# Kernel tuning notes

Hardware: AMD Instinct MI355X
Metric: run time of the kernel (lower is better)

The kernel has to match this reference:

```python
import jax, jax.numpy as jnp
import numpy as np

D = 1024        # model dim (== moe_inter_dim, required by Expert's x2*x3)
H = 1024        # expert hidden dim (moe_inter_dim)
E = 8           # n_routed_experts
K = 2           # n_activated_experts (top-k)
I = 2 * 1024    # shared-expert inter dim = n_shared_experts * moe_inter_dim
ROUTE_SCALE = 1.0


def setup_inputs() -> dict:
    key = jax.random.key(0)
    ks = jax.random.split(key, 12)
    s = lambda *sh: 1.0 / np.sqrt(sh[-1])
    return {
        "x":      jax.random.normal(ks[0], (1, 2048, D), jnp.float32),
        "gate_w": jax.random.normal(ks[1], (E, D), jnp.float32) * s(E, D),
        "w1":     jax.random.normal(ks[2], (E, H, D), jnp.float32) * s(H, D),
        "b1":     jax.random.normal(ks[3], (E, H), jnp.float32) * 0.01,
        "w2":     jax.random.normal(ks[4], (E, D, H), jnp.float32) * s(D, H),
        "b2":     jax.random.normal(ks[5], (E, D), jnp.float32) * 0.01,
        "w3":     jax.random.normal(ks[6], (E, H, D), jnp.float32) * s(H, D),
        "b3":     jax.random.normal(ks[7], (E, H), jnp.float32) * 0.01,
        "sw1":    jax.random.normal(ks[8], (I, D), jnp.float32) * s(I, D),
        "sw2":    jax.random.normal(ks[9], (I, D), jnp.float32) * s(I, D),
        "sw3":    jax.random.normal(ks[10], (D, I), jnp.float32) * s(D, I),
    }


def reference(x, gate_w, w1, b1, w2, b2, w3, b3, sw1, sw2, sw3):
    B, S, _ = x.shape
    xt = x.reshape(-1, D)                                  # (T, D)
    # ---- Gate (softmax scoring, n_groups==1, no bias, route_scale=1) ----
    logits = xt @ gate_w.T                                 # (T, E)
    scores = jax.nn.softmax(logits.astype(jnp.float32), axis=-1)
    top_vals, idx = jax.lax.top_k(scores, K)               # (T, K)
    weights = (jnp.take_along_axis(scores, idx, axis=1)
               .astype(x.dtype)) * ROUTE_SCALE             # (T, K)
    # ---- Routed experts: input is scaled by routing weight BEFORE expert ----
    xs = xt[:, None, :] * weights[:, :, None]              # (T, K, D)
    y = jnp.zeros_like(xt)
    for e in range(E):  # fixed small loop over experts (dense masked dispatch)
        mask = (idx == e).astype(x.dtype)                  # (T, K)
        h = jax.nn.silu(jnp.einsum('tkd,hd->tkh', xs, w1[e]) + b1[e])
        x2 = jnp.einsum('tkh,dh->tkd', h, w2[e]) + b2[e]   # (T, K, D)
        x3 = jnp.einsum('tkd,hd->tkh', xs, w3[e]) + b3[e]  # (T, K, H==D)
        y = y + jnp.sum((x2 * x3) * mask[:, :, None], axis=1)
    # ---- Shared experts (SwiGLU MLP, no biases) ----
    z = (jax.nn.silu(xt @ sw1.T) * (xt @ sw2.T)) @ sw3.T   # (T, D)
    return (y + z).reshape(B, S, D)
```

## Files before the change

### kernel.cpp

```cpp
#include <hip/hip_runtime.h>

typedef unsigned short u16;
typedef __attribute__((ext_vector_type(4))) float floatx4;
typedef __attribute__((ext_vector_type(8))) short short8;

#define MAXROWS 5120
#define MAXMT 40

__device__ __forceinline__ u16 f2bf(float f) {
    union { float f; unsigned u; } v; v.f = f;
    unsigned r = v.u + 0x7FFF + ((v.u >> 16) & 1);
    return (u16)(r >> 16);
}
__device__ __forceinline__ float bf2f(u16 h) {
    union { unsigned u; float f; } v; v.u = ((unsigned)h) << 16; return v.f;
}
__device__ __forceinline__ float silu_f(float x) { return x / (1.f + __expf(-x)); }

__device__ __forceinline__ void gl_lds16(const void* g, void* l) {
    __builtin_amdgcn_global_load_lds(
        (__attribute__((address_space(1))) unsigned int*)g,
        (__attribute__((address_space(3))) unsigned int*)l, 16, 0, 0);
}

__global__ void conv_gate(const float* __restrict__ w1, const float* __restrict__ w2,
                          const float* __restrict__ w3, const float* __restrict__ sw1,
                          const float* __restrict__ sw2, const float* __restrict__ sw3,
                          const float* __restrict__ x, const float* __restrict__ gw,
                          u16* __restrict__ W13, u16* __restrict__ W2b,
                          u16* __restrict__ S12, u16* __restrict__ S3b,
                          u16* __restrict__ Xb,
                          int* __restrict__ idxA, float* __restrict__ wA) {
    int bid = blockIdx.x;
    if (bid < 512) {
        int w = threadIdx.x >> 6, lane = threadIdx.x & 63;
        int t = bid * 4 + w;
        const float* xr = x + (size_t)t * 1024;
        float acc[8];
#pragma unroll
        for (int e = 0; e < 8; e++) acc[e] = 0.f;
#pragma unroll
        for (int i = 0; i < 16; i++) {
            float xv = xr[lane + (i << 6)];
#pragma unroll
            for (int e = 0; e < 8; e++) acc[e] += xv * gw[e * 1024 + lane + (i << 6)];
        }
#pragma unroll
        for (int e = 0; e < 8; e++)
            for (int off = 32; off > 0; off >>= 1) acc[e] += __shfl_xor(acc[e], off);
        if (lane == 0) {
            float m = acc[0];
#pragma unroll
            for (int e = 1; e < 8; e++) m = fmaxf(m, acc[e]);
            float p[8], s = 0.f;
#pragma unroll
            for (int e = 0; e < 8; e++) { p[e] = __expf(acc[e] - m); s += p[e]; }
            float inv = 1.f / s;
#pragma unroll
            for (int e = 0; e < 8; e++) p[e] *= inv;
            int i0 = 0;
#pragma unroll
            for (int e = 1; e < 8; e++) if (p[e] > p[i0]) i0 = e;
            int i1 = (i0 == 0) ? 1 : 0;
            for (int e = i1 + 1; e < 8; e++) if (e != i0 && p[e] > p[i1]) i1 = e;
            idxA[2 * t] = i0; idxA[2 * t + 1] = i1;
            wA[2 * t] = p[i0]; wA[2 * t + 1] = p[i1];
        }
        return;
    }
    long j = (long)(bid - 512) * 256 + threadIdx.x;
    const float* src; u16* dst; long d;
    if (j < 2097152) {
        long e = j >> 18; src = w1; dst = W13; d = j + (e << 18);
    } else if ((j -= 2097152) < 2097152) {
        long e = j >> 18; src = w3; dst = W13; d = j + (e << 18) + 262144;
    } else if ((j -= 2097152) < 2097152) { src = w2;  dst = W2b; d = j; }
    else if ((j -= 2097152) < 524288) {
        long rr = j >> 8, c4 = j & 255;
        long br = ((rr >> 4) << 5) + (rr & 15);
        src = sw1; dst = S12; d = (br << 8) + c4;
    } else if ((j -= 524288) < 524288) {
        long rr = j >> 8, c4 = j & 255;
        long br = ((rr >> 4) << 5) + 16 + (rr & 15);
        src = sw2; dst = S12; d = (br << 8) + c4;
    } else if ((j -= 524288) < 524288)     { src = sw3; dst = S3b; d = j; }
    else { j -= 524288; src = x; dst = Xb; d = j; }
    float4 v = ((const float4*)src)[j];
    ushort4 o; o.x = f2bf(v.x); o.y = f2bf(v.y); o.z = f2bf(v.z); o.w = f2bf(v.w);
    ((ushort4*)dst)[d] = o;
}

__global__ void rank_k(const int* __restrict__ idxA, int* __restrict__ tileexp,
                       int* __restrict__ ntiles, int* __restrict__ slot_of) {
    int lane = threadIdx.x;
    const int* my = idxA + lane * 64;
    int h[8];
#pragma unroll
    for (int e = 0; e < 8; e++) h[e] = 0;
    for (int i = 0; i < 64; i++) {
        int v = my[i];
#pragma unroll
        for (int e = 0; e < 8; e++) h[e] += (v == e);
    }
    int excl[8], tot[8];
#pragma unroll
    for (int e = 0; e < 8; e++) {
        int inc = h[e];
        for (int off = 1; off < 64; off <<= 1) {
            int up = __shfl_up(inc, off);
            if (lane >= off) inc += up;
        }
        excl[e] = inc - h[e];
        tot[e] = __shfl(inc, 63);
    }
    int base[8], tiles = 0;
#pragma unroll
    for (int e = 0; e < 8; e++) {
        base[e] = tiles * 128;
        tiles += (tot[e] + 127) >> 7;
    }
    if (lane == 0) {
        ntiles[0] = tiles;
        int t = 0;
        for (int e = 0; e < 8; e++) {
            int te = (tot[e] + 127) >> 7;
            for (int j = 0; j < te; j++) tileexp[t++] = e;
        }
    }
    int c[8];
#pragma unroll
    for (int e = 0; e < 8; e++) c[e] = base[e] + excl[e];
    for (int i = 0; i < 64; i++) {
        int v = my[i], slot = 0;
#pragma unroll
        for (int e = 0; e < 8; e++) slot += (v == e) ? c[e] : 0;
#pragma unroll
        for (int e = 0; e < 8; e++) c[e] += (v == e);
        slot_of[lane * 64 + i] = slot;
    }
}

__global__ void build_xs(const float* __restrict__ x, const float* __restrict__ wA,
                         const int* __restrict__ slot_of, u16* __restrict__ XS) {
    int s = blockIdx.x, i = threadIdx.x;
    int t = s >> 1; float w = wA[s]; int slot = slot_of[s];
    float4 v = ((const float4*)(x + (size_t)t * 1024))[i];
    ushort4 o; o.x = f2bf(v.x * w); o.y = f2bf(v.y * w); o.z = f2bf(v.z * w); o.w = f2bf(v.w * w);
    ((ushort4*)(XS + (size_t)slot * 1024))[i] = o;
}

#define STAGE64(Ab, Bb, lda)                                                        \
    {                                                                               \
        _Pragma("unroll")                                                           \
        for (int t = 0; t < 2; t++) {                                               \
            int b = w + (t << 2);                                                   \
            int r = (b << 4) + rloc;                                                \
            int cg = clds ^ ((r >> 1) & 3);                                         \
            _Pragma("unroll")                                                       \
            for (int hh = 0; hh < 2; hh++) {                                        \
                gl_lds16(Ab + (size_t)(m0 + r) * lda + k0 + (hh << 5) + (cg << 3),  \
                         &ldsA[(b * 2 + hh) * 512]);                                \
                gl_lds16(Bb + (size_t)(n0 + r) * lda + k0 + (hh << 5) + (cg << 3),  \
                         &ldsB[(b * 2 + hh) * 512]);                                \
            }                                                                       \
        }                                                                           \
    }

#define MFMA64()                                                                    \
    {                                                                               \
        _Pragma("unroll")                                                           \
        for (int hh = 0; hh < 2; hh++) {                                            \
            short8 af[4], bf[4];                                                    \
            _Pragma("unroll")                                                       \
            for (int i = 0; i < 4; i++) {                                           \
                int rr = (wm << 6) + (i << 4) + l15;                                \
                int g = q ^ ((rr >> 1) & 3);                                        \
                af[i] = *(const short8*)&ldsA[((rr >> 4) * 2 + hh) * 512 +          \
                                              (rr & 15) * 32 + (g << 3)];           \
            }                                                                       \
            _Pragma("unroll")                                                       \
            for (int j = 0; j < 4; j++) {                                           \
                int rr = (wn << 6) + (j << 4) + l15;                                \
                int g = q ^ ((rr >> 1) & 3);                                        \
                bf[j] = *(const short8*)&ldsB[((rr >> 4) * 2 + hh) * 512 +          \
                                              (rr & 15) * 32 + (g << 3)];           \
            }                                                                       \
            _Pragma("unroll")                                                       \
            for (int i = 0; i < 4; i++)                                             \
                _Pragma("unroll")                                                   \
                for (int j = 0; j < 4; j++)                                         \
                    acc[i][j] = __builtin_amdgcn_mfma_f32_16x16x32_bf16(            \
                        af[i], bf[j], acc[i][j], 0, 0, 0);                          \
        }                                                                           \
    }

__global__ __launch_bounds__(256) void gemm_A(
    const u16* __restrict__ XS, const u16* __restrict__ Xb,
    const u16* __restrict__ W13, const u16* __restrict__ S12,
    const float* __restrict__ b1, const float* __restrict__ b3,
    u16* __restrict__ H, u16* __restrict__ X3h, u16* __restrict__ G,
    const int* __restrict__ tileexp, const int* __restrict__ ntiles) {
    __shared__ u16 ldsA[128 * 64];
    __shared__ u16 ldsB[128 * 64];
    int xcd = blockIdx.x & 7, ws = blockIdx.x >> 3;
    const u16 *Ab, *Bb; int mt, nt, e = 0; bool routed;
    if (ws < 80) {
        routed = true;
        mt = xcd * 5 + (ws >> 4);
        nt = ws & 15;
        if (mt >= ntiles[0]) return;
        e = tileexp[mt];
        Ab = XS; Bb = W13 + ((size_t)e << 21);
    } else {
        routed = false; int s = ws - 80;
        mt = ((xcd >> 2) << 3) + (s >> 3);
        nt = ((xcd & 3) << 3) + (s & 7);
        Ab = Xb; Bb = S12;
    }
    int m0 = mt * 128, n0 = nt * 128;
    int tid = threadIdx.x, w = tid >> 6, lane = tid & 63;
    int wm = w >> 1, wn = w & 1;

    floatx4 acc[4][4];
#pragma unroll
    for (int i = 0; i < 4; i++)
#pragma unroll
        for (int j = 0; j < 4; j++) { floatx4 z = {0.f, 0.f, 0.f, 0.f}; acc[i][j] = z; }

    int rloc = lane >> 2, clds = lane & 3, q = lane >> 4, l15 = lane & 15;

    for (int k0 = 0; k0 < 1024; k0 += 64) {
        STAGE64(Ab, Bb, 1024);
        __syncthreads();
        MFMA64();
        __syncthreads();
    }

    if (routed) {
#pragma unroll
        for (int i = 0; i < 4; i++) {
            int rowb = m0 + (wm << 6) + (i << 4) + (q << 2);
#pragma unroll
            for (int j = 0; j < 4; j++) {
                int col = n0 + (wn << 6) + (j << 4) + l15;
#pragma unroll
                for (int r = 0; r < 4; r++) {
                    float v = acc[i][j][r];
                    int rw = rowb + r;
                    if (nt < 8) {
                        H[(size_t)rw * 1024 + col] = f2bf(silu_f(v + b1[e * 1024 + col]));
                    } else {
                        int c2 = col - 1024;
                        X3h[(size_t)rw * 1024 + c2] = f2bf(v + b3[e * 1024 + c2]);
                    }
                }
            }
        }
    } else {
#pragma unroll
        for (int i = 0; i < 4; i++) {
            int rowb = m0 + (wm << 6) + (i << 4) + (q << 2);
#pragma unroll
            for (int jp = 0; jp < 4; jp += 2) {
                int brb = n0 + (wn << 6) + (jp << 4);
                int lcol = ((brb >> 5) << 4) + l15;
#pragma unroll
                for (int r = 0; r < 4; r++) {
                    float u = acc[i][jp][r], v = acc[i][jp + 1][r];
                    G[(size_t)(rowb + r) * 2048 + lcol] = f2bf(silu_f(u) * v);
                }
            }
        }
    }
}

__global__ __launch_bounds__(256) void gemm_B(
    const u16* __restrict__ H, const u16* __restrict__ G,
    const u16* __restrict__ W2b, const u16* __restrict__ S3b,
    const float* __restrict__ b2, const u16* __restrict__ X3h,
    u16* __restrict__ P0, u16* __restrict__ P1,
    float* __restrict__ Z0, float* __restrict__ Z1,
    const int* __restrict__ tileexp, const int* __restrict__ ntiles) {
    __shared__ u16 ldsA[128 * 64];
    __shared__ u16 ldsB[128 * 64];
    int xcd = blockIdx.x & 7, ws = blockIdx.x >> 3;
    const u16 *Ab, *Bb; int mt, nt, kc, lda, kbeg, kspan, e = 0; bool routed;
    if (ws < 80) {
        routed = true;
        mt = xcd * 5 + (ws >> 4);
        int r = ws & 15; nt = r & 7; kc = r >> 3;
        if (mt >= ntiles[0]) return;
        e = tileexp[mt];
        Ab = H; Bb = W2b + ((size_t)e << 20); lda = 1024; kbeg = kc << 9; kspan = 512;
    } else {
        routed = false; int s = ws - 80;
        kc = s & 1; int s2 = s >> 1;
        mt = ((xcd >> 1) << 2) + (s2 >> 2);
        nt = ((xcd & 1) << 2) + (s2 & 3);
        Ab = G; Bb = S3b; lda = 2048; kbeg = kc << 10; kspan = 1024;
    }
    int kend = kbeg + kspan;
    int m0 = mt * 128, n0 = nt * 128;
    int tid = threadIdx.x, w = tid >> 6, lane = tid & 63;
    int wm = w >> 1, wn = w & 1;

    floatx4 acc[4][4];
#pragma unroll
    for (int i = 0; i < 4; i++)
#pragma unroll
        for (int j = 0; j < 4; j++) { floatx4 z = {0.f, 0.f, 0.f, 0.f}; acc[i][j] = z; }

    int rloc = lane >> 2, clds = lane & 3, q = lane >> 4, l15 = lane & 15;

    for (int k0 = kbeg; k0 < kend; k0 += 64) {
        STAGE64(Ab, Bb, lda);
        __syncthreads();
        MFMA64();
        __syncthreads();
    }

    if (routed) {
        u16* Pk = kc ? P1 : P0;
#pragma unroll
        for (int i = 0; i < 4; i++) {
            int rowb = m0 + (wm << 6) + (i << 4) + (q << 2);
#pragma unroll
            for (int j = 0; j < 4; j++) {
                int col = n0 + (wn << 6) + (j << 4) + l15;
#pragma unroll
                for (int r = 0; r < 4; r++) {
                    int rw = rowb + r;
                    float v = acc[i][j][r] + (kc == 0 ? b2[e * 1024 + col] : 0.f);
                    float pv = v * bf2f(X3h[(size_t)rw * 1024 + col]);
                    Pk[(size_t)rw * 1024 + col] = f2bf(pv);
                }
            }
        }
    } else {
        float* Zk = kc ? Z1 : Z0;
#pragma unroll
        for (int i = 0; i < 4; i++) {
            int rowb = m0 + (wm << 6) + (i << 4) + (q << 2);
#pragma unroll
            for (int j = 0; j < 4; j++) {
                int col = n0 + (wn << 6) + (j << 4) + l15;
#pragma unroll
                for (int r = 0; r < 4; r++)
                    Zk[(size_t)(rowb + r) * 1024 + col] = acc[i][j][r];
            }
        }
    }
}

__global__ void final_k(const float* __restrict__ Z0, const float* __restrict__ Z1,
                        const u16* __restrict__ P0, const u16* __restrict__ P1,
                        const int* __restrict__ slot_of, float* __restrict__ out) {
    int i = blockIdx.x * 256 + threadIdx.x;
    int t = i >> 8, c4 = i & 255;
    int s0 = slot_of[2 * t], s1 = slot_of[2 * t + 1];
    float4 z0 = ((const float4*)Z0)[(size_t)t * 256 + c4];
    float4 z1 = ((const float4*)Z1)[(size_t)t * 256 + c4];
    ushort4 a0 = ((const ushort4*)P0)[(size_t)s0 * 256 + c4];
    ushort4 a1 = ((const ushort4*)P1)[(size_t)s0 * 256 + c4];
    ushort4 c0 = ((const ushort4*)P0)[(size_t)s1 * 256 + c4];
    ushort4 c1 = ((const ushort4*)P1)[(size_t)s1 * 256 + c4];
    float4 o;
    o.x = z0.x + z1.x + bf2f(a0.x) + bf2f(a1.x) + bf2f(c0.x) + bf2f(c1.x);
    o.y = z0.y + z1.y + bf2f(a0.y) + bf2f(a1.y) + bf2f(c0.y) + bf2f(c1.y);
    o.z = z0.z + z1.z + bf2f(a0.z) + bf2f(a1.z) + bf2f(c0.z) + bf2f(c1.z);
    o.w = z0.w + z1.w + bf2f(a0.w) + bf2f(a1.w) + bf2f(c0.w) + bf2f(c1.w);
    ((float4*)out)[(size_t)t * 256 + c4] = o;
}

extern "C" void kernel_launch(void* const* d_in, const int* in_sizes, int n_in,
                              void* d_out, int out_size, void* d_ws, size_t ws_size,
                              hipStream_t stream) {
    const float* x   = (const float*)d_in[0];
    const float* gw  = (const float*)d_in[1];
    const float* w1  = (const float*)d_in[2];
    const float* b1  = (const float*)d_in[3];
    const float* w2  = (const float*)d_in[4];
    const float* b2  = (const float*)d_in[5];
    const float* w3  = (const float*)d_in[6];
    const float* b3  = (const float*)d_in[7];
    const float* sw1 = (const float*)d_in[8];
    const float* sw2 = (const float*)d_in[9];
    const float* sw3 = (const float*)d_in[10];
    float* out = (float*)d_out;

    char* p = (char*)d_ws;
    int* ntiles  = (int*)(p + 192);
    int* tileexp = (int*)(p + 256);
    size_t off = 4096;
    u16*   XS      = (u16*)(p + off);   off += (size_t)MAXROWS * 1024 * 2;
    int*   idxA    = (int*)(p + off);   off += 16384;
    float* wA      = (float*)(p + off); off += 16384;
    int*   slot_of = (int*)(p + off);   off += 16384;
    u16*   H       = (u16*)(p + off);   off += (size_t)MAXROWS * 1024 * 2;
    u16*   X3h     = (u16*)(p + off);   off += (size_t)MAXROWS * 1024 * 2;
    u16*   P0      = (u16*)(p + off);   off += (size_t)MAXROWS * 1024 * 2;
    u16*   P1      = (u16*)(p + off);   off += (size_t)MAXROWS * 1024 * 2;
    float* Z0      = (float*)(p + off); off += (size_t)2048 * 1024 * 4;
    float* Z1      = (float*)(p + off); off += (size_t)2048 * 1024 * 4;
    u16*   W13     = (u16*)(p + off);   off += (size_t)8 * 2048 * 1024 * 2;
    u16*   W2b     = (u16*)(p + off);   off += (size_t)8 * 1024 * 1024 * 2;
    u16*   S12     = (u16*)(p + off);   off += (size_t)4096 * 1024 * 2;
    u16*   S3b     = (u16*)(p + off);   off += (size_t)1024 * 2048 * 2;
    u16*   Xb      = (u16*)(p + off);   off += (size_t)2048 * 1024 * 2;
    u16*   G       = (u16*)(p + off);   off += (size_t)2048 * 2048 * 2;

    conv_gate<<<33280, 256, 0, stream>>>(w1, w2, w3, sw1, sw2, sw3, x, gw,
                                         W13, W2b, S12, S3b, Xb, idxA, wA);
    rank_k<<<1, 64, 0, stream>>>(idxA, tileexp, ntiles, slot_of);
    build_xs<<<4096, 256, 0, stream>>>(x, wA, slot_of, XS);

    gemm_A<<<1152, 256, 0, stream>>>(XS, Xb, W13, S12, b1, b3, H, X3h, G,
                                     tileexp, ntiles);
    gemm_B<<<896, 256, 0, stream>>>(H, G, W2b, S3b, b2, X3h, P0, P1, Z0, Z1,
                                    tileexp, ntiles);
    final_k<<<2048, 256, 0, stream>>>(Z0, Z1, P0, P1, slot_of, out);
}
```

Before: 316.1 us.

## Double-buffer LDS staging of K=32 slices to overlap global loads with MFMA

Replaces the single-buffer K=64 stage/compute loop in both GEMM kernels with a two-buffer K=32 pipeline. The next slice is issued via global_load_lds while the current one feeds MFMAs, using explicit vmcnt waits and raw barriers. Fragment reads are done in inline asm with precomputed LDS addresses and a single lgkmcnt wait. LDS footprint stays at 32 KB, but barriers per K-step increase, and the hand-coded waitcnt values must match the number of in-flight loads.

```diff
diff --git a/kernel.cpp b/kernel.cpp
--- a/kernel.cpp
+++ b/kernel.cpp
@@ -22,6 +22,31 @@
         (__attribute__((address_space(1))) unsigned int*)g,
         (__attribute__((address_space(3))) unsigned int*)l, 16, 0, 0);
 }
+
+__device__ __forceinline__ void ld_frags(
+    unsigned a0, unsigned a1, unsigned a2, unsigned a3,
+    unsigned b0, unsigned b1, unsigned b2, unsigned b3,
+    short8& af0, short8& af1, short8& af2, short8& af3,
+    short8& bf0, short8& bf1, short8& bf2, short8& bf3) {
+    asm volatile(
+        "ds_read_b128 %0, %8\n\t"
+        "ds_read_b128 %1, %9\n\t"
+        "ds_read_b128 %2, %10\n\t"
+        "ds_read_b128 %3, %11\n\t"
+        "ds_read_b128 %4, %12\n\t"
+        "ds_read_b128 %5, %13\n\t"
+        "ds_read_b128 %6, %14\n\t"
+        "ds_read_b128 %7, %15\n\t"
+        "s_waitcnt lgkmcnt(0)"
+        : "=&v"(af0), "=&v"(af1), "=&v"(af2), "=&v"(af3),
+          "=&v"(bf0), "=&v"(bf1), "=&v"(bf2), "=&v"(bf3)
+        : "v"(a0), "v"(a1), "v"(a2), "v"(a3),
+          "v"(b0), "v"(b1), "v"(b2), "v"(b3));
+}
+
+#define WAIT_VM4() __builtin_amdgcn_s_waitcnt(3956)
+#define WAIT_VM0() __builtin_amdgcn_s_waitcnt(3952)
+#define BAR()      __builtin_amdgcn_s_barrier()
 
 __global__ void conv_gate(const float* __restrict__ w1, const float* __restrict__ w2,
                           const float* __restrict__ w3, const float* __restrict__ sw1,
@@ -149,50 +174,81 @@
     ((ushort4*)(XS + (size_t)slot * 1024))[i] = o;
 }
 
-#define STAGE64(Ab, Bb, lda)                                                        \
-    {                                                                               \
-        _Pragma("unroll")                                                           \
-        for (int t = 0; t < 2; t++) {                                               \
-            int b = w + (t << 2);                                                   \
-            int r = (b << 4) + rloc;                                                \
-            int cg = clds ^ ((r >> 1) & 3);                                         \
-            _Pragma("unroll")                                                       \
-            for (int hh = 0; hh < 2; hh++) {                                        \
-                gl_lds16(Ab + (size_t)(m0 + r) * lda + k0 + (hh << 5) + (cg << 3),  \
-                         &ldsA[(b * 2 + hh) * 512]);                                \
-                gl_lds16(Bb + (size_t)(n0 + r) * lda + k0 + (hh << 5) + (cg << 3),  \
-                         &ldsB[(b * 2 + hh) * 512]);                                \
-            }                                                                       \
-        }                                                                           \
-    }
-
-#define MFMA64()                                                                    \
-    {                                                                               \
-        _Pragma("unroll")                                                           \
-        for (int hh = 0; hh < 2; hh++) {                                            \
-            short8 af[4], bf[4];                                                    \
-            _Pragma("unroll")                                                       \
-            for (int i = 0; i < 4; i++) {                                           \
-                int rr = (wm << 6) + (i << 4) + l15;                                \
-                int g = q ^ ((rr >> 1) & 3);                                        \
-                af[i] = *(const short8*)&ldsA[((rr >> 4) * 2 + hh) * 512 +          \
-                                              (rr & 15) * 32 + (g << 3)];           \
-            }                                                                       \
-            _Pragma("unroll")                                                       \
-            for (int j = 0; j < 4; j++) {                                           \
-                int rr = (wn << 6) + (j << 4) + l15;                                \
-                int g = q ^ ((rr >> 1) & 3);                                        \
-                bf[j] = *(const short8*)&ldsB[((rr >> 4) * 2 + hh) * 512 +          \
-                                              (rr & 15) * 32 + (g << 3)];           \
-            }                                                                       \
-            _Pragma("unroll")                                                       \
-            for (int i = 0; i < 4; i++)                                             \
-                _Pragma("unroll")                                                   \
-                for (int j = 0; j < 4; j++)                                         \
-                    acc[i][j] = __builtin_amdgcn_mfma_f32_16x16x32_bf16(            \
-                        af[i], bf[j], acc[i][j], 0, 0, 0);                          \
-        }                                                                           \
-    }
+#define STAGE32(BUF, Ab, Bb, lda, kk)                                          \
+    {                                                                          \
+        _Pragma("unroll")                                                      \
+        for (int t = 0; t < 2; t++) {                                          \
+            int r = (w << 4) + (t << 6) + rloc;                                \
+            int cg = clds ^ ((r >> 1) & 3);                                    \
+            gl_lds16(Ab + (size_t)(m0 + r) * (lda) + (kk) + (cg << 3),         \
+                     LDS + (BUF)*4096 + ((w << 4) + (t << 6)) * 32);           \
+            gl_lds16(Bb + (size_t)(n0 + r) * (lda) + (kk) + (cg << 3),         \
+                     LDS + 8192 + (BUF)*4096 + ((w << 4) + (t << 6)) * 32);    \
+        }                                                                      \
+    }
+
+#define COMPUTE32(BUF)                                                         \
+    {                                                                          \
+        short8 af[4], bf[4];                                                   \
+        ld_frags(adA[0] + (BUF)*8192, adA[1] + (BUF)*8192,                     \
+                 adA[2] + (BUF)*8192, adA[3] + (BUF)*8192,                     \
+                 adB[0] + (BUF)*8192, adB[1] + (BUF)*8192,                     \
+                 adB[2] + (BUF)*8192, adB[3] + (BUF)*8192,                     \
+                 af[0], af[1], af[2], af[3], bf[0], bf[1], bf[2], bf[3]);      \
+        _Pragma("unroll")                                                      \
+        for (int i = 0; i < 4; i++)                                            \
+            _Pragma("unroll")                                                  \
+            for (int j = 0; j < 4; j++)                                        \
+                acc[i][j] = __builtin_amdgcn_mfma_f32_16x16x32_bf16(           \
+                    af[i], bf[j], acc[i][j], 0, 0, 0);                         \
+    }
+
+#define KLOOP(NP, Ab, Bb, lda, kbeg)                                           \
+    {                                                                          \
+        STAGE32(0, Ab, Bb, lda, (kbeg));                                       \
+        for (int ii = 0; ii < (NP); ii++) {                                    \
+            int kk = (kbeg) + (ii << 6);                                       \
+            STAGE32(1, Ab, Bb, lda, kk + 32);                                  \
+            WAIT_VM4(); BAR();                                                 \
+            COMPUTE32(0);                                                      \
+            BAR();                                                             \
+            if (ii + 1 < (NP)) {                                               \
+                STAGE32(0, Ab, Bb, lda, kk + 64);                              \
+                WAIT_VM4();                                                    \
+            } else {                                                           \
+                WAIT_VM0();                                                    \
+            }                                                                  \
+            BAR();                                                             \
+            COMPUTE32(1);                                                      \
+            BAR();                                                             \
+        }                                                                      \
+    }
+
+#define GEMM_PRE()                                                             \
+    int tid = threadIdx.x, w = tid >> 6, lane = tid & 63;                      \
+    int wm = w >> 1, wn = w & 1;                                               \
+    int rloc = lane >> 2, clds = lane & 3, q = lane >> 4, l15 = lane & 15;     \
+    unsigned ldsbase = (unsigned)(size_t)(__attribute__((address_space(3))) u16*)LDS; \
+    unsigned adA[4], adB[4];                                                   \
+    _Pragma("unroll")                                                          \
+    for (int i = 0; i < 4; i++) {                                              \
+        int rr = (wm << 6) + (i << 4) + l15;                                   \
+        int g = q ^ ((rr >> 1) & 3);                                           \
+        adA[i] = ldsbase + rr * 64 + g * 16;                                   \
+    }                                                                          \
+    _Pragma("unroll")                                                          \
+    for (int j = 0; j < 4; j++) {                                              \
+        int rr = (wn << 6) + (j << 4) + l15;                                   \
+        int g = q ^ ((rr >> 1) & 3);                                           \
+        adB[j] = ldsbase + 16384 + rr * 64 + g * 16;                           \
+    }                                                                          \
+    floatx4 acc[4][4];                                                         \
+    _Pragma("unroll")                                                          \
+    for (int i = 0; i < 4; i++)                                                \
+        _Pragma("unroll")                                                      \
+        for (int j = 0; j < 4; j++) {                                          \
+            floatx4 z = {0.f, 0.f, 0.f, 0.f}; acc[i][j] = z;                   \
+        }
 
 __global__ __launch_bounds__(256) void gemm_A(
     const u16* __restrict__ XS, const u16* __restrict__ Xb,
@@ -200,8 +256,7 @@
     const float* __restrict__ b1, const float* __restrict__ b3,
     u16* __restrict__ H, u16* __restrict__ X3h, u16* __restrict__ G,
     const int* __restrict__ tileexp, const int* __restrict__ ntiles) {
-    __shared__ u16 ldsA[128 * 64];
-    __shared__ u16 ldsB[128 * 64];
+    __shared__ u16 LDS[16384];
     int xcd = blockIdx.x & 7, ws = blockIdx.x >> 3;
     const u16 *Ab, *Bb; int mt, nt, e = 0; bool routed;
     if (ws < 80) {
@@ -218,23 +273,9 @@
         Ab = Xb; Bb = S12;
     }
     int m0 = mt * 128, n0 = nt * 128;
-    int tid = threadIdx.x, w = tid >> 6, lane = tid & 63;
-    int wm = w >> 1, wn = w & 1;
-
-    floatx4 acc[4][4];
-#pragma unroll
-    for (int i = 0; i < 4; i++)
-#pragma unroll
-        for (int j = 0; j < 4; j++) { floatx4 z = {0.f, 0.f, 0.f, 0.f}; acc[i][j] = z; }
-
-    int rloc = lane >> 2, clds = lane & 3, q = lane >> 4, l15 = lane & 15;
-
-    for (int k0 = 0; k0 < 1024; k0 += 64) {
-        STAGE64(Ab, Bb, 1024);
-        __syncthreads();
-        MFMA64();
-        __syncthreads();
-    }
+    GEMM_PRE();
+
+    KLOOP(16, Ab, Bb, 1024, 0);
 
     if (routed) {
 #pragma unroll
@@ -281,43 +322,27 @@
     u16* __restrict__ P0, u16* __restrict__ P1,
     float* __restrict__ Z0, float* __restrict__ Z1,
     const int* __restrict__ tileexp, const int* __restrict__ ntiles) {
-    __shared__ u16 ldsA[128 * 64];
-    __shared__ u16 ldsB[128 * 64];
+    __shared__ u16 LDS[16384];
     int xcd = blockIdx.x & 7, ws = blockIdx.x >> 3;
-    const u16 *Ab, *Bb; int mt, nt, kc, lda, kbeg, kspan, e = 0; bool routed;
+    const u16 *Ab, *Bb; int mt, nt, kc, lda, kbeg, np, e = 0; bool routed;
     if (ws < 80) {
         routed = true;
         mt = xcd * 5 + (ws >> 4);
         int r = ws & 15; nt = r & 7; kc = r >> 3;
         if (mt >= ntiles[0]) return;
         e = tileexp[mt];
-        Ab = H; Bb = W2b + ((size_t)e << 20); lda = 1024; kbeg = kc << 9; kspan = 512;
+        Ab = H; Bb = W2b + ((size_t)e << 20); lda = 1024; kbeg = kc << 9; np = 8;
     } else {
         routed = false; int s = ws - 80;
         kc = s & 1; int s2 = s >> 1;
         mt = ((xcd >> 1) << 2) + (s2 >> 2);
         nt = ((xcd & 1) << 2) + (s2 & 3);
-        Ab = G; Bb = S3b; lda = 2048; kbeg = kc << 10; kspan = 1024;
-    }
-    int kend = kbeg + kspan;
+        Ab = G; Bb = S3b; lda = 2048; kbeg = kc << 10; np = 16;
+    }
     int m0 = mt * 128, n0 = nt * 128;
-    int tid = threadIdx.x, w = tid >> 6, lane = tid & 63;
-    int wm = w >> 1, wn = w & 1;
-
-    floatx4 acc[4][4];
-#pragma unroll
-    for (int i = 0; i < 4; i++)
-#pragma unroll
-        for (int j = 0; j < 4; j++) { floatx4 z = {0.f, 0.f, 0.f, 0.f}; acc[i][j] = z; }
-
-    int rloc = lane >> 2, clds = lane & 3, q = lane >> 4, l15 = lane & 15;
-
-    for (int k0 = kbeg; k0 < kend; k0 += 64) {
-        STAGE64(Ab, Bb, lda);
-        __syncthreads();
-        MFMA64();
-        __syncthreads();
-    }
+    GEMM_PRE();
+
+    KLOOP(np, Ab, Bb, lda, kbeg);
 
     if (routed) {
         u16* Pk = kc ? P1 : P0;
```

Result: no change. 310.7 us (-1.7%).
